# Kernel optimization log

Measured on AMD Instinct MI355X. Metric: run time of the kernel, lower is better.

## Reference

```python
import jax, jax.numpy as jnp
import numpy as np


def _conv(x, w, pad):
    return jax.lax.conv_general_dilated(
        x, w, (1, 1), [(pad, pad), (pad, pad)],
        dimension_numbers=('NCHW', 'OIHW', 'NCHW'))


def _avgpool2(x):
    B, C, H, W = x.shape
    return x.reshape(B, C, H // 2, 2, W // 2, 2).mean(axis=(3, 5))


def setup_inputs() -> dict:
    key = jax.random.key(0)
    ks = jax.random.split(key, 10)
    B = 1024
    x = jax.random.uniform(ks[0], (B, 1, 28, 28), jnp.float32)
    # depthwise-separable conv params (in=1 -> depthwise is a plain 3x3 conv)
    dw_w = jax.random.normal(ks[1], (1, 1, 3, 3), jnp.float32) * 0.3
    pw_w = jax.random.normal(ks[2], (32, 1, 1, 1), jnp.float32) * 0.3
    pw_b = jax.random.normal(ks[3], (32,), jnp.float32) * 0.05
    # fixed 4-qubit entangling unitary (real orthogonal 16x16), stand-in for tq.RandomLayer(n_ops=8)
    U = jnp.asarray(np.linalg.qr(np.random.default_rng(0).standard_normal((16, 16)))[0],
                    jnp.float32)
    fus_w = jax.random.normal(ks[4], (128, 36, 3, 3), jnp.float32) * (1.0 / np.sqrt(36 * 9))
    fus_b = jax.random.normal(ks[5], (128,), jnp.float32) * 0.05
    F = 128 * 7 * 7
    cls_w = jax.random.normal(ks[6], (10, F), jnp.float32) * (1.0 / np.sqrt(F))
    cls_b = jax.random.normal(ks[7], (10,), jnp.float32) * 0.05
    reg_w = jax.random.normal(ks[8], (1, F), jnp.float32) * (1.0 / np.sqrt(F))
    reg_b = jax.random.normal(ks[9], (1,), jnp.float32) * 0.05
    return {'x': x, 'dw_w': dw_w, 'pw_w': pw_w, 'pw_b': pw_b, 'U': U,
            'fus_w': fus_w, 'fus_b': fus_b, 'cls_w': cls_w, 'cls_b': cls_b,
            'reg_w': reg_w, 'reg_b': reg_b}


def _quantum_patches(x, U):
    # x: (B,1,28,28) -> 14x14 grid of 2x2 patches, 4 RY angles per patch
    B = x.shape[0]
    p = x.reshape(B, 14, 2, 14, 2).transpose(0, 1, 3, 2, 4).reshape(B, 14, 14, 4)
    h = 0.5 * p
    a = jnp.stack([jnp.cos(h), jnp.sin(h)], axis=-1)       # (B,14,14,4,2)
    # RY-encoded product state |psi> = kron over 4 wires -> 16 real amplitudes
    amp = jnp.einsum('...i,...j,...k,...l->...ijkl',
                     a[..., 0, :], a[..., 1, :], a[..., 2, :], a[..., 3, :]
                     ).reshape(B, 14, 14, 16)
    state = amp @ U.T                                       # entangling layer
    probs = state * state
    idx = jnp.arange(16)
    # PauliZ expectation per wire; wire 0 is the most significant bit
    signs = 1.0 - 2.0 * (((idx[None, :] >> (3 - jnp.arange(4)[:, None])) & 1)
                         .astype(jnp.float32))              # (4,16)
    meas = probs @ signs.T                                  # (B,14,14,4)
    # replicate torch.cat(patches,dim=1).view(B,4,14,14): flat row-major then reshape
    return meas.reshape(B, 14 * 14 * 4).reshape(B, 4, 14, 14)


def reference(x, dw_w, pw_w, pw_b, U, fus_w, fus_b, cls_w, cls_b, reg_w, reg_b):
    B = x.shape[0]
    out_ds = _conv(_conv(x, dw_w, 1), pw_w, 0) + pw_b[None, :, None, None]  # (B,32,28,28)
    out_q = _quantum_patches(x, U)                                          # (B,4,14,14)
    out = jnp.concatenate([_avgpool2(out_ds), out_q], axis=1)               # (B,36,14,14)
    out = jax.nn.relu(_conv(out, fus_w, 1) + fus_b[None, :, None, None])    # (B,128,14,14)
    out = _avgpool2(out)                                                    # (B,128,7,7)
    flat = out.reshape(B, -1)
    logits = flat @ cls_w.T + cls_b
    aux = flat @ reg_w.T + reg_b
    return (logits, aux)
```

## Files before the change

### kernel.cpp

```cpp
#include <hip/hip_runtime.h>
#include <math.h>


typedef __bf16 bf16x8 __attribute__((ext_vector_type(8)));
typedef float  f32x16 __attribute__((ext_vector_type(16)));

union Pack8 { __bf16 h[8]; uint4 v; };

__global__ __launch_bounds__(256) void prep(
    const float* __restrict__ fus_w,
    const float* __restrict__ cls_w,
    const float* __restrict__ reg_w,
    __bf16* __restrict__ bfrag,
    float* __restrict__ clsTT)
{
    const int gid = blockIdx.x * 256 + threadIdx.x;
    if (gid < 55296) {
        const int j    = gid & 7;
        const int frag = gid >> 3;
        const int lane = frag & 63;
        const int rest = frag >> 6;
        const int m  = rest % 27;
        const int nt = rest / 27;
        const int t  = m / 3, ks = m - t * 3;
        const int n  = nt * 32 + (lane & 31);
        const int ic = ks * 16 + (lane >> 5) * 8 + j;
        const float v = (ic < 36) ? fus_w[n * 324 + ic * 9 + t] : 0.f;
        bfrag[gid] = (__bf16)v;
    } else if (gid < 55296 + 86016) {
        const int e   = gid - 55296;
        const int kk  = e % 12;
        const int r0  = e / 12;
        const int l31 = r0 & 31;
        const int r1  = r0 >> 5;
        const int hk  = r1 & 1;
        const int r2  = r1 >> 1;
        const int q   = r2 & 3;
        const int r3  = r2 >> 2;
        const int mt  = r3 % 7;
        const int nt  = r3 / 7;
        const int oc   = nt * 32 + l31;
        const int cell = mt * 8 + q * 2 + hk;
        float v = 0.f;
        if (cell < 49 && kk < 11) {
            const int f = oc * 49 + cell;
            v = (kk < 10) ? cls_w[kk * 6272 + f] : reg_w[f];
        }
        clsTT[e] = v;
    }
}

__global__ __launch_bounds__(256, 3) void quanv_fused(
    const float* __restrict__ x,
    const float* __restrict__ dw_w,
    const float* __restrict__ pw_w,
    const float* __restrict__ pw_b,
    const float* __restrict__ U,
    const __bf16* __restrict__ bfrag,
    const float* __restrict__ fus_b,
    const float* __restrict__ clsTT,
    const float* __restrict__ cls_b,
    const float* __restrict__ reg_b,
    float* __restrict__ out,
    int B)
{
    __shared__ __align__(16) __bf16 actT[256 * 56];
    __shared__ float xs[784];
    __shared__ float red[48];

    const int b   = blockIdx.x;
    const int tid = threadIdx.x;
    const float* xb = x + b * 784;

    {
        uint4 z; z.x = 0; z.y = 0; z.z = 0; z.w = 0;
        for (int i = tid; i < 1792; i += 256) ((uint4*)actT)[i] = z;
        for (int i = tid; i < 784; i += 256) xs[i] = xb[i];
    }
    __syncthreads();

    if (tid < 196) {
        const int i = tid / 14, j = tid % 14;
        const int Y = 2 * i, X = 2 * j;

        float w9[9];
        #pragma unroll
        for (int t = 0; t < 9; ++t) w9[t] = dw_w[t];
        float dsum = 0.f;
        #pragma unroll
        for (int dy = 0; dy < 2; ++dy) {
            #pragma unroll
            for (int dx = 0; dx < 2; ++dx) {
                const int cy = Y + dy, cx = X + dx;
                #pragma unroll
                for (int ky = 0; ky < 3; ++ky) {
                    const int yy = cy + ky - 1;
                    if (yy < 0 || yy > 27) continue;
                    #pragma unroll
                    for (int kx = 0; kx < 3; ++kx) {
                        const int xx = cx + kx - 1;
                        if (xx < 0 || xx > 27) continue;
                        dsum += xs[yy * 28 + xx] * w9[ky * 3 + kx];
                    }
                }
            }
        }
        const float dpool = 0.25f * dsum;

        const int sp_o = (i + 1) * 16 + (j + 1);
        #pragma unroll
        for (int c8 = 0; c8 < 4; ++c8) {
            Pack8 pk;
            #pragma unroll
            for (int e = 0; e < 8; ++e)
                pk.h[e] = (__bf16)(pw_w[c8 * 8 + e] * dpool + pw_b[c8 * 8 + e]);
            ((uint4*)actT)[sp_o * 7 + c8] = pk.v;
        }

        const float p0 = xs[Y * 28 + X],       p1 = xs[Y * 28 + X + 1];
        const float p2 = xs[(Y + 1) * 28 + X], p3 = xs[(Y + 1) * 28 + X + 1];
        float c0, s0, c1, s1, c2, s2, c3, s3;
        sincosf(0.5f * p0, &s0, &c0);
        sincosf(0.5f * p1, &s1, &c1);
        sincosf(0.5f * p2, &s2, &c2);
        sincosf(0.5f * p3, &s3, &c3);
        float a01[4] = {c0 * c1, c0 * s1, s0 * c1, s0 * s1};
        float a23[4] = {c2 * c3, c2 * s3, s2 * c3, s2 * s3};
        float amp[16];
        #pragma unroll
        for (int hi = 0; hi < 4; ++hi)
            #pragma unroll
            for (int lo = 0; lo < 4; ++lo)
                amp[hi * 4 + lo] = a01[hi] * a23[lo];

        float meas[4] = {0.f, 0.f, 0.f, 0.f};
        #pragma unroll
        for (int m = 0; m < 16; ++m) {
            float st = 0.f;
            #pragma unroll
            for (int n = 0; n < 16; ++n) st = fmaf(U[m * 16 + n], amp[n], st);
            const float pm = st * st;
            meas[0] += ((m >> 3) & 1) ? -pm : pm;
            meas[1] += ((m >> 2) & 1) ? -pm : pm;
            meas[2] += ((m >> 1) & 1) ? -pm : pm;
            meas[3] += (m & 1) ? -pm : pm;
        }
        const int fbase = i * 56 + j * 4;
        #pragma unroll
        for (int w = 0; w < 4; ++w) {
            const int f  = fbase + w;
            const int ch = f / 196;
            const int sp = f - ch * 196;
            const int r2 = sp / 14 + 1, c2i = sp % 14 + 1;
            const int sp2 = r2 * 16 + c2i;
            actT[sp2 * 56 + 32 + ch] = (__bf16)meas[w];
        }
    }
    __syncthreads();

    const int lane = tid & 63, nt = tid >> 6;
    const int l31  = lane & 31, hk = lane >> 5;
    const float fb_l = fus_b[nt * 32 + l31];

    bf16x8 bfr[27];
    {
        const bf16x8* __restrict__ bp = ((const bf16x8*)bfrag) + (nt * 27 * 64 + lane);
        #pragma unroll
        for (int m = 0; m < 27; ++m) bfr[m] = bp[m * 64];
    }

    float a11[11];
    #pragma unroll
    for (int k = 0; k < 11; ++k) a11[k] = 0.f;

    const float4* __restrict__ cls4 =
        ((const float4*)clsTT) + ((((nt * 7) * 4) * 2 + hk) * 32 + l31) * 3;

    for (int mt = 0; mt < 7; ++mt) {
        const int mp   = mt * 32 + l31;
        int cell = mp >> 2;
        const int cc = (cell < 49) ? cell : 48;
        const int py = (cc * 9363) >> 16;
        const int px = cc - py * 7;
        const int yy = 2 * py + ((mp >> 1) & 1);
        const int xx = 2 * px + (mp & 1);
        const int rowbase = yy * 16 + xx;

        f32x16 acc = {0.f,0.f,0.f,0.f,0.f,0.f,0.f,0.f,
                      0.f,0.f,0.f,0.f,0.f,0.f,0.f,0.f};

        #pragma unroll
        for (int t = 0; t < 9; ++t) {
            const int ky = t / 3, kx = t - ky * 3;
            const int row = rowbase + ky * 16 + kx;
            const __bf16* rp = actT + row * 56 + hk * 8;
            #pragma unroll
            for (int ks = 0; ks < 3; ++ks) {
                const bf16x8 af = *(const bf16x8*)(rp + ks * 16);
                acc = __builtin_amdgcn_mfma_f32_32x32x16_bf16(af, bfr[t * 3 + ks],
                                                              acc, 0, 0, 0);
            }
        }

        const float4* cwm = cls4 + mt * (4 * 2 * 32 * 3);
        #pragma unroll
        for (int q = 0; q < 4; ++q) {
            float pv = 0.f;
            #pragma unroll
            for (int s = 0; s < 4; ++s) {
                const float v = acc[q * 4 + s] + fb_l;
                pv += (v > 0.f ? v : 0.f);
            }
            pv *= 0.25f;
            const float4 w0 = cwm[q * 192 + 0];
            const float4 w1 = cwm[q * 192 + 1];
            const float4 w2 = cwm[q * 192 + 2];
            a11[0]  = fmaf(pv, w0.x, a11[0]);
            a11[1]  = fmaf(pv, w0.y, a11[1]);
            a11[2]  = fmaf(pv, w0.z, a11[2]);
            a11[3]  = fmaf(pv, w0.w, a11[3]);
            a11[4]  = fmaf(pv, w1.x, a11[4]);
            a11[5]  = fmaf(pv, w1.y, a11[5]);
            a11[6]  = fmaf(pv, w1.z, a11[6]);
            a11[7]  = fmaf(pv, w1.w, a11[7]);
            a11[8]  = fmaf(pv, w2.x, a11[8]);
            a11[9]  = fmaf(pv, w2.y, a11[9]);
            a11[10] = fmaf(pv, w2.z, a11[10]);
        }
    }
    __syncthreads();

    const int wv = tid >> 6;
    #pragma unroll
    for (int k = 0; k < 11; ++k) {
        float a = a11[k];
        #pragma unroll
        for (int off = 32; off > 0; off >>= 1) a += __shfl_down(a, off, 64);
        if (lane == 0) red[k * 4 + wv] = a;
    }
    __syncthreads();
    if (tid < 11) {
        const float v = red[tid * 4] + red[tid * 4 + 1] + red[tid * 4 + 2] + red[tid * 4 + 3];
        if (tid < 10) out[b * 10 + tid] = v + cls_b[tid];
        else          out[B * 10 + b]   = v + reg_b[0];
    }
}

extern "C" void kernel_launch(void* const* d_in, const int* in_sizes, int n_in,
                              void* d_out, int out_size, void* d_ws, size_t ws_size,
                              hipStream_t stream) {
    const float* x    = (const float*)d_in[0];
    const float* dw_w = (const float*)d_in[1];
    const float* pw_w = (const float*)d_in[2];
    const float* pw_b = (const float*)d_in[3];
    const float* U    = (const float*)d_in[4];
    const float* fw   = (const float*)d_in[5];
    const float* fb   = (const float*)d_in[6];
    const float* cw   = (const float*)d_in[7];
    const float* cb   = (const float*)d_in[8];
    const float* rw   = (const float*)d_in[9];
    const float* rb   = (const float*)d_in[10];
    const int B = in_sizes[0] / 784;

    __bf16* bfrag = (__bf16*)d_ws;
    float*  clsTT = (float*)((char*)d_ws + 110592);

    prep<<<(55296 + 86016 + 255) / 256, 256, 0, stream>>>(fw, cw, rw, bfrag, clsTT);
    quanv_fused<<<B, 256, 0, stream>>>(x, dw_w, pw_w, pw_b, U, bfrag, fb,
                                       clsTT, cb, rb, (float*)d_out, B);
}
```

Measured before the change: 122.3 us.

## Process two images per block, overlapping patch work with MFMA conv

Each block now handles two batch images. The bf16 weight fragments are loaded into registers once and reused for both images, and the second image's quantum/depthwise patch stage runs alongside the first image's MFMA convolution and classifier fold. This aims to amortize the per-block fragment loads and hide the scalar patch stage behind tensor work. The cost is double the shared memory, a launch bound lowered to 2 blocks per CU, and only 512 blocks for a batch of 1024, which may reduce latency hiding. Within a wave the patch and conv code still run one after the other; the overlap comes from different waves being in different phases.

```diff
diff --git a/kernel.cpp b/kernel.cpp
--- a/kernel.cpp
+++ b/kernel.cpp
@@ -50,135 +50,97 @@
     }
 }
 
-__global__ __launch_bounds__(256, 3) void quanv_fused(
-    const float* __restrict__ x,
-    const float* __restrict__ dw_w,
-    const float* __restrict__ pw_w,
-    const float* __restrict__ pw_b,
-    const float* __restrict__ U,
-    const __bf16* __restrict__ bfrag,
-    const float* __restrict__ fus_b,
-    const float* __restrict__ clsTT,
-    const float* __restrict__ cls_b,
-    const float* __restrict__ reg_b,
-    float* __restrict__ out,
-    int B)
+__device__ __forceinline__ void patch_work(
+    const int tid, const float* __restrict__ xs, __bf16* __restrict__ actT,
+    const float* __restrict__ dw_w, const float* __restrict__ pw_w,
+    const float* __restrict__ pw_b, const float* __restrict__ U)
 {
-    __shared__ __align__(16) __bf16 actT[256 * 56];
-    __shared__ float xs[784];
-    __shared__ float red[48];
-
-    const int b   = blockIdx.x;
-    const int tid = threadIdx.x;
-    const float* xb = x + b * 784;
-
-    {
-        uint4 z; z.x = 0; z.y = 0; z.z = 0; z.w = 0;
-        for (int i = tid; i < 1792; i += 256) ((uint4*)actT)[i] = z;
-        for (int i = tid; i < 784; i += 256) xs[i] = xb[i];
-    }
-    __syncthreads();
-
-    if (tid < 196) {
-        const int i = tid / 14, j = tid % 14;
-        const int Y = 2 * i, X = 2 * j;
-
-        float w9[9];
-        #pragma unroll
-        for (int t = 0; t < 9; ++t) w9[t] = dw_w[t];
-        float dsum = 0.f;
-        #pragma unroll
-        for (int dy = 0; dy < 2; ++dy) {
+    if (tid >= 196) return;
+    const int i = tid / 14, j = tid % 14;
+    const int Y = 2 * i, X = 2 * j;
+
+    float w9[9];
+    #pragma unroll
+    for (int t = 0; t < 9; ++t) w9[t] = dw_w[t];
+    float dsum = 0.f;
+    #pragma unroll
+    for (int dy = 0; dy < 2; ++dy) {
+        #pragma unroll
+        for (int dx = 0; dx < 2; ++dx) {
+            const int cy = Y + dy, cx = X + dx;
             #pragma unroll
-            for (int dx = 0; dx < 2; ++dx) {
-                const int cy = Y + dy, cx = X + dx;
+            for (int ky = 0; ky < 3; ++ky) {
+                const int yy = cy + ky - 1;
+                if (yy < 0 || yy > 27) continue;
                 #pragma unroll
-                for (int ky = 0; ky < 3; ++ky) {
-                    const int yy = cy + ky - 1;
-                    if (yy < 0 || yy > 27) continue;
-                    #pragma unroll
-                    for (int kx = 0; kx < 3; ++kx) {
-                        const int xx = cx + kx - 1;
-                        if (xx < 0 || xx > 27) continue;
-                        dsum += xs[yy * 28 + xx] * w9[ky * 3 + kx];
-                    }
+                for (int kx = 0; kx < 3; ++kx) {
+                    const int xx = cx + kx - 1;
+                    if (xx < 0 || xx > 27) continue;
+                    dsum += xs[yy * 28 + xx] * w9[ky * 3 + kx];
                 }
             }
         }
-        const float dpool = 0.25f * dsum;
-
-        const int sp_o = (i + 1) * 16 + (j + 1);
-        #pragma unroll
-        for (int c8 = 0; c8 < 4; ++c8) {
-            Pack8 pk;
-            #pragma unroll
-            for (int e = 0; e < 8; ++e)
-                pk.h[e] = (__bf16)(pw_w[c8 * 8 + e] * dpool + pw_b[c8 * 8 + e]);
-            ((uint4*)actT)[sp_o * 7 + c8] = pk.v;
-        }
-
-        const float p0 = xs[Y * 28 + X],       p1 = xs[Y * 28 + X + 1];
-        const float p2 = xs[(Y + 1) * 28 + X], p3 = xs[(Y + 1) * 28 + X + 1];
-        float c0, s0, c1, s1, c2, s2, c3, s3;
-        sincosf(0.5f * p0, &s0, &c0);
-        sincosf(0.5f * p1, &s1, &c1);
-        sincosf(0.5f * p2, &s2, &c2);
-        sincosf(0.5f * p3, &s3, &c3);
-        float a01[4] = {c0 * c1, c0 * s1, s0 * c1, s0 * s1};
-        float a23[4] = {c2 * c3, c2 * s3, s2 * c3, s2 * s3};
-        float amp[16];
-        #pragma unroll
-        for (int hi = 0; hi < 4; ++hi)
-            #pragma unroll
-            for (int lo = 0; lo < 4; ++lo)
-                amp[hi * 4 + lo] = a01[hi] * a23[lo];
-
-        float meas[4] = {0.f, 0.f, 0.f, 0.f};
-        #pragma unroll
-        for (int m = 0; m < 16; ++m) {
-            float st = 0.f;
-            #pragma unroll
-            for (int n = 0; n < 16; ++n) st = fmaf(U[m * 16 + n], amp[n], st);
-            const float pm = st * st;
-            meas[0] += ((m >> 3) & 1) ? -pm : pm;
-            meas[1] += ((m >> 2) & 1) ? -pm : pm;
-            meas[2] += ((m >> 1) & 1) ? -pm : pm;
-            meas[3] += (m & 1) ? -pm : pm;
-        }
-        const int fbase = i * 56 + j * 4;
-        #pragma unroll
-        for (int w = 0; w < 4; ++w) {
-            const int f  = fbase + w;
-            const int ch = f / 196;
-            const int sp = f - ch * 196;
-            const int r2 = sp / 14 + 1, c2i = sp % 14 + 1;
-            const int sp2 = r2 * 16 + c2i;
-            actT[sp2 * 56 + 32 + ch] = (__bf16)meas[w];
-        }
-    }
-    __syncthreads();
-
-    const int lane = tid & 63, nt = tid >> 6;
-    const int l31  = lane & 31, hk = lane >> 5;
-    const float fb_l = fus_b[nt * 32 + l31];
-
-    bf16x8 bfr[27];
-    {
-        const bf16x8* __restrict__ bp = ((const bf16x8*)bfrag) + (nt * 27 * 64 + lane);
-        #pragma unroll
-        for (int m = 0; m < 27; ++m) bfr[m] = bp[m * 64];
-    }
-
-    float a11[11];
-    #pragma unroll
-    for (int k = 0; k < 11; ++k) a11[k] = 0.f;
-
-    const float4* __restrict__ cls4 =
-        ((const float4*)clsTT) + ((((nt * 7) * 4) * 2 + hk) * 32 + l31) * 3;
-
+    }
+    const float dpool = 0.25f * dsum;
+
+    const int sp_o = (i + 1) * 16 + (j + 1);
+    #pragma unroll
+    for (int c8 = 0; c8 < 4; ++c8) {
+        Pack8 pk;
+        #pragma unroll
+        for (int e = 0; e < 8; ++e)
+            pk.h[e] = (__bf16)(pw_w[c8 * 8 + e] * dpool + pw_b[c8 * 8 + e]);
+        ((uint4*)actT)[sp_o * 7 + c8] = pk.v;
+    }
+
+    const float p0 = xs[Y * 28 + X],       p1 = xs[Y * 28 + X + 1];
+    const float p2 = xs[(Y + 1) * 28 + X], p3 = xs[(Y + 1) * 28 + X + 1];
+    float c0, s0, c1, s1, c2, s2, c3, s3;
+    sincosf(0.5f * p0, &s0, &c0);
+    sincosf(0.5f * p1, &s1, &c1);
+    sincosf(0.5f * p2, &s2, &c2);
+    sincosf(0.5f * p3, &s3, &c3);
+    float a01[4] = {c0 * c1, c0 * s1, s0 * c1, s0 * s1};
+    float a23[4] = {c2 * c3, c2 * s3, s2 * c3, s2 * s3};
+    float amp[16];
+    #pragma unroll
+    for (int hi = 0; hi < 4; ++hi)
+        #pragma unroll
+        for (int lo = 0; lo < 4; ++lo)
+            amp[hi * 4 + lo] = a01[hi] * a23[lo];
+
+    float meas[4] = {0.f, 0.f, 0.f, 0.f};
+    #pragma unroll
+    for (int m = 0; m < 16; ++m) {
+        float st = 0.f;
+        #pragma unroll
+        for (int n = 0; n < 16; ++n) st = fmaf(U[m * 16 + n], amp[n], st);
+        const float pm = st * st;
+        meas[0] += ((m >> 3) & 1) ? -pm : pm;
+        meas[1] += ((m >> 2) & 1) ? -pm : pm;
+        meas[2] += ((m >> 1) & 1) ? -pm : pm;
+        meas[3] += (m & 1) ? -pm : pm;
+    }
+    const int fbase = i * 56 + j * 4;
+    #pragma unroll
+    for (int w = 0; w < 4; ++w) {
+        const int f  = fbase + w;
+        const int ch = f / 196;
+        const int sp = f - ch * 196;
+        const int r2 = sp / 14 + 1, c2i = sp % 14 + 1;
+        const int sp2 = r2 * 16 + c2i;
+        actT[sp2 * 56 + 32 + ch] = (__bf16)meas[w];
+    }
+}
+
+__device__ __forceinline__ void conv_fold(
+    const __bf16* __restrict__ actT, const bf16x8* __restrict__ bfr,
+    const float4* __restrict__ cls4, const float fb_l,
+    const int l31, const int hk, float* __restrict__ a11)
+{
     for (int mt = 0; mt < 7; ++mt) {
         const int mp   = mt * 32 + l31;
-        int cell = mp >> 2;
+        const int cell = mp >> 2;
         const int cc = (cell < 49) ? cell : 48;
         const int py = (cc * 9363) >> 16;
         const int px = cc - py * 7;
@@ -202,7 +164,7 @@
             }
         }
 
-        const float4* cwm = cls4 + mt * (4 * 2 * 32 * 3);
+        const float4* cwm = cls4 + mt * 768;
         #pragma unroll
         for (int q = 0; q < 4; ++q) {
             float pv = 0.f;
@@ -228,21 +190,95 @@
             a11[10] = fmaf(pv, w2.z, a11[10]);
         }
     }
+}
+
+__global__ __launch_bounds__(256, 2) void quanv_fused(
+    const float* __restrict__ x,
+    const float* __restrict__ dw_w,
+    const float* __restrict__ pw_w,
+    const float* __restrict__ pw_b,
+    const float* __restrict__ U,
+    const __bf16* __restrict__ bfrag,
+    const float* __restrict__ fus_b,
+    const float* __restrict__ clsTT,
+    const float* __restrict__ cls_b,
+    const float* __restrict__ reg_b,
+    float* __restrict__ out,
+    int B)
+{
+    __shared__ __align__(16) __bf16 actT[2][256 * 56];
+    __shared__ float xs[2][784];
+    __shared__ float red[2][48];
+
+    const int b0  = blockIdx.x * 2;
+    const int b1  = b0 + 1;
+    const bool two = (b1 < B);
+    const int tid = threadIdx.x;
+
+    {
+        uint4 z; z.x = 0; z.y = 0; z.z = 0; z.w = 0;
+        uint4* a4 = (uint4*)&actT[0][0];
+        for (int i = tid; i < 3584; i += 256) a4[i] = z;
+        const float* xb = x + (size_t)b0 * 784;
+        const int tot = two ? 1568 : 784;
+        float* xf = &xs[0][0];
+        for (int i = tid; i < tot; i += 256) xf[i] = xb[i];
+    }
+
+    const int lane = tid & 63, nt = tid >> 6;
+    const int l31  = lane & 31, hk = lane >> 5;
+    const float fb_l = fus_b[nt * 32 + l31];
+
+    bf16x8 bfr[27];
+    {
+        const bf16x8* __restrict__ bp = ((const bf16x8*)bfrag) + (nt * 27 * 64 + lane);
+        #pragma unroll
+        for (int m = 0; m < 27; ++m) bfr[m] = bp[m * 64];
+    }
+
+    const float4* __restrict__ cls4 =
+        ((const float4*)clsTT) + ((((nt * 7) * 4) * 2 + hk) * 32 + l31) * 3;
+
     __syncthreads();
 
-    const int wv = tid >> 6;
+    patch_work(tid, &xs[0][0], &actT[0][0], dw_w, pw_w, pw_b, U);
+    __syncthreads();
+
+    float a11_0[11];
+    #pragma unroll
+    for (int k = 0; k < 11; ++k) a11_0[k] = 0.f;
+    if (two) patch_work(tid, &xs[1][0], &actT[1][0], dw_w, pw_w, pw_b, U);
+    conv_fold(&actT[0][0], bfr, cls4, fb_l, l31, hk, a11_0);
+    __syncthreads();
+
+    float a11_1[11];
+    #pragma unroll
+    for (int k = 0; k < 11; ++k) a11_1[k] = 0.f;
+    if (two) conv_fold(&actT[1][0], bfr, cls4, fb_l, l31, hk, a11_1);
+
     #pragma unroll
     for (int k = 0; k < 11; ++k) {
-        float a = a11[k];
-        #pragma unroll
-        for (int off = 32; off > 0; off >>= 1) a += __shfl_down(a, off, 64);
-        if (lane == 0) red[k * 4 + wv] = a;
+        float a = a11_0[k];
+        float c = a11_1[k];
+        #pragma unroll
+        for (int off = 32; off > 0; off >>= 1) {
+            a += __shfl_down(a, off, 64);
+            c += __shfl_down(c, off, 64);
+        }
+        if (lane == 0) { red[0][k * 4 + nt] = a; red[1][k * 4 + nt] = c; }
     }
     __syncthreads();
     if (tid < 11) {
-        const float v = red[tid * 4] + red[tid * 4 + 1] + red[tid * 4 + 2] + red[tid * 4 + 3];
-        if (tid < 10) out[b * 10 + tid] = v + cls_b[tid];
-        else          out[B * 10 + b]   = v + reg_b[0];
+        const float v = red[0][tid * 4] + red[0][tid * 4 + 1]
+                      + red[0][tid * 4 + 2] + red[0][tid * 4 + 3];
+        if (tid < 10) out[b0 * 10 + tid] = v + cls_b[tid];
+        else          out[B * 10 + b0]   = v + reg_b[0];
+    } else if (two && tid >= 64 && tid < 75) {
+        const int k = tid - 64;
+        const float v = red[1][k * 4] + red[1][k * 4 + 1]
+                      + red[1][k * 4 + 2] + red[1][k * 4 + 3];
+        if (k < 10) out[b1 * 10 + k] = v + cls_b[k];
+        else        out[B * 10 + b1] = v + reg_b[0];
     }
 }
 
@@ -266,6 +302,7 @@
     float*  clsTT = (float*)((char*)d_ws + 110592);
 
     prep<<<(55296 + 86016 + 255) / 256, 256, 0, stream>>>(fw, cw, rw, bfrag, clsTT);
-    quanv_fused<<<B, 256, 0, stream>>>(x, dw_w, pw_w, pw_b, U, bfrag, fb,
-                                       clsTT, cb, rb, (float*)d_out, B);
-}
+    const int nblk = (B + 1) / 2;
+    quanv_fused<<<nblk, 256, 0, stream>>>(x, dw_w, pw_w, pw_b, U, bfrag, fb,
+                                          clsTT, cb, rb, (float*)d_out, B);
+}
```

After: 110.6 us. 1.11x faster.
